# Performance work log

Hardware: AMD Instinct MI355X
Metric: run time of the kernel (lower is better)

Reference implementation:

```python
import jax, jax.numpy as jnp
import numpy as np

N = 50000        # nodes
E = 1_600_000    # edges
IN = 64          # in_feats
H = 128          # h_feats
L = 5            # num_layers
G = 512          # graphs in batch
C = 10           # num_classes


def setup_inputs() -> dict:
    key = jax.random.key(0)
    ks = jax.random.split(key, 12)
    s = 0.05
    x = jax.random.normal(ks[0], (N, IN), jnp.float32)
    edge_index = jax.random.randint(ks[1], (2, E), 0, N, dtype=jnp.int32)
    batch = jnp.sort(jax.random.randint(ks[2], (N,), 0, G, dtype=jnp.int32))
    edge_weight = jax.random.uniform(ks[3], (E,), jnp.float32)
    # GatedGraphConv params: per-layer mixing weight + shared GRUCell
    weight = jax.random.normal(ks[4], (L, H, H), jnp.float32) * s
    w_ih = jax.random.normal(ks[5], (3 * H, H), jnp.float32) * s
    w_hh = jax.random.normal(ks[6], (3 * H, H), jnp.float32) * s
    b_ih = jax.random.normal(ks[7], (3 * H,), jnp.float32) * s
    b_hh = jax.random.normal(ks[8], (3 * H,), jnp.float32) * s
    # MLP head
    dense1_w = jax.random.normal(ks[9], (4 * H, H), jnp.float32) * s
    dense1_b = jnp.zeros((4 * H,), jnp.float32)
    dense2_w = jax.random.normal(ks[10], (C, 4 * H), jnp.float32) * s
    dense2_b = jnp.zeros((C,), jnp.float32)
    return dict(x=x, edge_index=edge_index, batch=batch, edge_weight=edge_weight,
                weight=weight, w_ih=w_ih, w_hh=w_hh, b_ih=b_ih, b_hh=b_hh,
                dense1_w=dense1_w, dense1_b=dense1_b,
                dense2_w=dense2_w, dense2_b=dense2_b)


def _gru_cell(m, h, w_ih, w_hh, b_ih, b_hh):
    # torch.nn.GRUCell(input=m, hidden=h)
    gi = m @ w_ih.T + b_ih
    gh = h @ w_hh.T + b_hh
    i_r, i_z, i_n = jnp.split(gi, 3, axis=-1)
    h_r, h_z, h_n = jnp.split(gh, 3, axis=-1)
    r = jax.nn.sigmoid(i_r + h_r)
    z = jax.nn.sigmoid(i_z + h_z)
    n = jnp.tanh(i_n + r * h_n)
    return (1.0 - z) * n + z * h


def reference(x, edge_index, batch, edge_weight, weight, w_ih, w_hh, b_ih, b_hh,
              dense1_w, dense1_b, dense2_w, dense2_b):
    src, dst = edge_index[0], edge_index[1]
    # pad in_feats -> h_feats (PyG GatedGraphConv)
    h = jnp.pad(x, ((0, 0), (0, H - IN)))
    for l in range(L):
        m = h @ weight[l]                          # [N, H]
        msg = m[src] * edge_weight[:, None]        # gather + edge gating [E, H]
        agg = jax.ops.segment_sum(msg, dst, num_segments=N)  # scatter-add
        h = _gru_cell(agg, h, w_ih, w_hh, b_ih, b_hh)
    pooled = jax.ops.segment_max(h, batch, num_segments=G)   # global max pool [G, H]
    # dropout is identity in eval mode
    hid = jax.nn.relu(pooled @ dense1_w.T + dense1_b)
    out = hid @ dense2_w.T + dense2_b
    return out
```

## Files before the change

### kernel.cpp

```cpp
#include <hip/hip_runtime.h>
#include <hip/hip_bf16.h>

#define NN 50000
#define NE 1600000
#define FIN 64
#define H 128
#define NL 5
#define NG 512
#define NC 10

typedef __attribute__((ext_vector_type(8))) short short8;
typedef __attribute__((ext_vector_type(4))) float f32x4;

#define OFF_H2A   0
#define OFF_H2B   3200000
#define OFF_CUR   6400000
#define OFF_OFF   6450176
#define OFF_CSR   6500352
#define OFF_POOL  8900352
#define OFF_FWF   8965888
#define OFF_FWHH  9088768

__device__ __forceinline__ short rne_bf16(float f){
    unsigned u = __float_as_uint(f);
    unsigned r = (u + 0x7FFFu + ((u >> 16) & 1u)) >> 16;
    return (short)r;
}
__device__ __forceinline__ float bf_lo(unsigned v){ return __uint_as_float(v << 16); }
__device__ __forceinline__ float bf_hi(unsigned v){ return __uint_as_float(v & 0xFFFF0000u); }


__global__ void k_hist(const int* __restrict__ ei, int* __restrict__ cnt){
    int e = blockIdx.x*256 + threadIdx.x;
    if (e < NE) atomicAdd(&cnt[ei[NE + e]], 1);
}

__global__ void k_scan(int* __restrict__ cur, int* __restrict__ off){
    __shared__ int s[1024];
    int t = threadIdx.x;
    const int CH = 49;
    int base = t*CH;
    int m = (NN + 1) - base; if (m > CH) m = CH; if (m < 0) m = 0;
    int sum = 0;
    for (int i = 0; i < m; ++i) sum += (cur[base + i] + 15) & ~15;
    s[t] = sum; __syncthreads();
    for (int o = 1; o < 1024; o <<= 1){
        int v = (t >= o) ? s[t - o] : 0; __syncthreads();
        s[t] += v; __syncthreads();
    }
    int run = s[t] - sum;
    for (int i = 0; i < m; ++i){
        int c = (cur[base + i] + 15) & ~15;
        off[base + i] = run;
        cur[base + i] = run;
        run += c;
    }
}

__global__ void k_fill(const int* __restrict__ ei, const float* __restrict__ ew,
                       int* __restrict__ cur, unsigned* __restrict__ csr){
    int e = blockIdx.x*256 + threadIdx.x;
    if (e >= NE) return;
    int src = ei[e], dst = ei[NE + e];
    int pos = atomicAdd(&cur[dst], 1);
    csr[pos] = (unsigned)src | (((unsigned)(ushort)rne_bf16(ew[e])) << 16);
}


__global__ void k_pad(const float* __restrict__ x, ushort* __restrict__ h2a){
    int idx = blockIdx.x*256 + threadIdx.x;
    int n = idx >> 4, f8 = idx & 15;
    short8 v;
    if (f8 < 8){
        float4 a = *(const float4*)(x + n*FIN + f8*8);
        float4 b = *(const float4*)(x + n*FIN + f8*8 + 4);
        v[0]=rne_bf16(a.x); v[1]=rne_bf16(a.y); v[2]=rne_bf16(a.z); v[3]=rne_bf16(a.w);
        v[4]=rne_bf16(b.x); v[5]=rne_bf16(b.y); v[6]=rne_bf16(b.z); v[7]=rne_bf16(b.w);
    } else {
        v[0]=0; v[1]=0; v[2]=0; v[3]=0; v[4]=0; v[5]=0; v[6]=0; v[7]=0;
    }
    *(short8*)(h2a + idx*8) = v;
}

__global__ void k_fuse(const float* __restrict__ W, const float* __restrict__ wih,
                       short* __restrict__ fwf){
    int idx = blockIdx.x*256 + threadIdx.x;
    int l = idx / 49152;
    int r = idx % 49152;
    int k = r / 384, n = r % 384;
    const float4* wl = (const float4*)(W + l*16384 + k*128);
    const float4* wi = (const float4*)(wih + n*128);
    float acc = 0.f;
    #pragma unroll 8
    for (int c = 0; c < 32; ++c){
        float4 a = wl[c], b = wi[c];
        acc += a.x*b.x + a.y*b.y + a.z*b.z + a.w*b.w;
    }
    int lane = ((k>>3)&3)*16 + (n&15);
    fwf[l*49152 + (((n>>4)*4 + (k>>5))*64 + lane)*8 + (k&7)] = rne_bf16(acc);
}

__global__ void k_cvt_whh(const float* __restrict__ whh, short* __restrict__ fwhh){
    int idx = blockIdx.x*256 + threadIdx.x;
    int k = idx / 384, n = idx % 384;
    float v = whh[n*128 + k];
    int lane = ((k>>3)&3)*16 + (n&15);
    fwhh[(((n>>4)*4 + (k>>5))*64 + lane)*8 + (k&7)] = rne_bf16(v);
}

__global__ void k_init_pool(unsigned* __restrict__ p){
    p[blockIdx.x*256 + threadIdx.x] = 0x007FFFFFu;
}

__global__ __launch_bounds__(512)
void k_layer(const ushort* __restrict__ h2r, ushort* __restrict__ h2w,
             const int* __restrict__ off, const unsigned* __restrict__ csr,
             const short* __restrict__ fwf, const short* __restrict__ fwhh,
             const float* __restrict__ b_ih, const float* __restrict__ b_hh,
             const int* __restrict__ batch, unsigned* __restrict__ pooled,
             int last){
    __shared__ ushort tl[16*136];
    int tid = threadIdx.x;
    int n0 = blockIdx.x * 16;
    int wave = tid >> 6, lane = tid & 63;
    int lane_lo = lane & 15, quad = lane >> 4;
    int grp = lane >> 4, fl = lane & 15;

    for (int sub = 0; sub < 2; ++sub){
        int node = n0 + wave*2 + sub;
        int start = __builtin_amdgcn_readfirstlane(off[node]);
        int end   = __builtin_amdgcn_readfirstlane(off[node + 1]);
        float a0=0.f,a1=0.f,a2=0.f,a3=0.f,a4=0.f,a5=0.f,a6=0.f,a7=0.f;
        const ushort* hb = h2r + fl*8;
        for (int i = start; i < end; i += 16){
            uint4 c = *(const uint4*)(csr + i + grp*4);
            uint4 v0 = *(const uint4*)(hb + (c.x & 0xFFFFu)*H);
            uint4 v1 = *(const uint4*)(hb + (c.y & 0xFFFFu)*H);
            uint4 v2 = *(const uint4*)(hb + (c.z & 0xFFFFu)*H);
            uint4 v3 = *(const uint4*)(hb + (c.w & 0xFFFFu)*H);
            float w0 = bf_hi(c.x), w1 = bf_hi(c.y), w2 = bf_hi(c.z), w3 = bf_hi(c.w);
            a0 += w0*bf_lo(v0.x); a1 += w0*bf_hi(v0.x); a2 += w0*bf_lo(v0.y); a3 += w0*bf_hi(v0.y);
            a4 += w0*bf_lo(v0.z); a5 += w0*bf_hi(v0.z); a6 += w0*bf_lo(v0.w); a7 += w0*bf_hi(v0.w);
            a0 += w1*bf_lo(v1.x); a1 += w1*bf_hi(v1.x); a2 += w1*bf_lo(v1.y); a3 += w1*bf_hi(v1.y);
            a4 += w1*bf_lo(v1.z); a5 += w1*bf_hi(v1.z); a6 += w1*bf_lo(v1.w); a7 += w1*bf_hi(v1.w);
            a0 += w2*bf_lo(v2.x); a1 += w2*bf_hi(v2.x); a2 += w2*bf_lo(v2.y); a3 += w2*bf_hi(v2.y);
            a4 += w2*bf_lo(v2.z); a5 += w2*bf_hi(v2.z); a6 += w2*bf_lo(v2.w); a7 += w2*bf_hi(v2.w);
            a0 += w3*bf_lo(v3.x); a1 += w3*bf_hi(v3.x); a2 += w3*bf_lo(v3.y); a3 += w3*bf_hi(v3.y);
            a4 += w3*bf_lo(v3.z); a5 += w3*bf_hi(v3.z); a6 += w3*bf_lo(v3.w); a7 += w3*bf_hi(v3.w);
        }
        a0 += __shfl_xor(a0,16); a1 += __shfl_xor(a1,16); a2 += __shfl_xor(a2,16); a3 += __shfl_xor(a3,16);
        a4 += __shfl_xor(a4,16); a5 += __shfl_xor(a5,16); a6 += __shfl_xor(a6,16); a7 += __shfl_xor(a7,16);
        a0 += __shfl_xor(a0,32); a1 += __shfl_xor(a1,32); a2 += __shfl_xor(a2,32); a3 += __shfl_xor(a3,32);
        a4 += __shfl_xor(a4,32); a5 += __shfl_xor(a5,32); a6 += __shfl_xor(a6,32); a7 += __shfl_xor(a7,32);
        if (lane < 16){
            short8 hbv;
            hbv[0]=rne_bf16(a0); hbv[1]=rne_bf16(a1); hbv[2]=rne_bf16(a2); hbv[3]=rne_bf16(a3);
            hbv[4]=rne_bf16(a4); hbv[5]=rne_bf16(a5); hbv[6]=rne_bf16(a6); hbv[7]=rne_bf16(a7);
            *(short8*)(tl + (wave*2 + sub)*136 + fl*8) = hbv;
        }
    }
    __syncthreads();

    f32x4 ai[3], ah[3];
    #pragma unroll
    for (int i = 0; i < 3; ++i){ ai[i] = (f32x4){0.f,0.f,0.f,0.f}; ah[i] = (f32x4){0.f,0.f,0.f,0.f}; }

    const ushort* arow_t = tl + lane_lo*136;
    const ushort* arow_h = h2r + (size_t)(n0 + lane_lo)*H;
    #pragma unroll
    for (int kt = 0; kt < 4; ++kt){
        short8 at  = *(const short8*)(arow_t + kt*32 + quad*8);
        short8 ahh = *(const short8*)(arow_h + kt*32 + quad*8);
        #pragma unroll
        for (int s = 0; s < 3; ++s){
            int tile = (s*8 + wave)*4 + kt;
            short8 bi = *(const short8*)(fwf  + tile*512 + lane*8);
            short8 bh = *(const short8*)(fwhh + tile*512 + lane*8);
            ai[s] = __builtin_amdgcn_mfma_f32_16x16x32_bf16(at,  bi, ai[s], 0, 0, 0);
            ah[s] = __builtin_amdgcn_mfma_f32_16x16x32_bf16(ahh, bh, ah[s], 0, 0, 0);
        }
    }

    {
        int j = wave*16 + lane_lo;
        float bir = b_ih[j], biz = b_ih[128 + j], bin_ = b_ih[256 + j];
        float bhr = b_hh[j], bhz = b_hh[128 + j], bhn  = b_hh[256 + j];
        #pragma unroll
        for (int r = 0; r < 4; ++r){
            int row = n0 + quad*4 + r;
            float gir = ai[0][r] + bir, ghr = ah[0][r] + bhr;
            float giz = ai[1][r] + biz, ghz = ah[1][r] + bhz;
            float gin = ai[2][r] + bin_, ghn = ah[2][r] + bhn;
            float rr = 1.f/(1.f + __expf(-(gir + ghr)));
            float zz = 1.f/(1.f + __expf(-(giz + ghz)));
            float nn = tanhf(gin + rr*ghn);
            float ho = __uint_as_float(((unsigned)h2r[(size_t)row*H + j]) << 16);
            float hv = (1.f - zz)*nn + zz*ho;
            if (!last){
                h2w[(size_t)row*H + j] = (ushort)rne_bf16(hv);
            } else {
                int g = batch[row];
                unsigned u = __float_as_uint(hv);
                u = (u & 0x80000000u) ? ~u : (u | 0x80000000u);
                atomicMax(pooled + g*H + j, u);
            }
        }
    }
}


__global__ void k_head(const unsigned* __restrict__ pooled,
                       const float* __restrict__ d1w, const float* __restrict__ d1b,
                       const float* __restrict__ d2w, const float* __restrict__ d2b,
                       float* __restrict__ out){
    __shared__ float sp[128];
    __shared__ float shid[512];
    int g = blockIdx.x, tid = threadIdx.x;
    if (tid < 128){
        unsigned u = pooled[g*H + tid];
        sp[tid] = __uint_as_float((u & 0x80000000u) ? (u ^ 0x80000000u) : ~u);
    }
    __syncthreads();
    for (int o = tid; o < 512; o += 256){
        float acc = d1b[o];
        for (int k = 0; k < H; ++k) acc += sp[k] * d1w[o*H + k];
        shid[o] = fmaxf(acc, 0.f);
    }
    __syncthreads();
    if (tid < NC){
        float acc = d2b[tid];
        for (int o = 0; o < 512; ++o) acc += shid[o] * d2w[tid*512 + o];
        out[g*NC + tid] = acc;
    }
}

extern "C" void kernel_launch(void* const* d_in, const int* in_sizes, int n_in,
                              void* d_out, int out_size, void* d_ws, size_t ws_size,
                              hipStream_t stream){
    const float* x     = (const float*)d_in[0];
    const int*   ei    = (const int*)d_in[1];
    const int*   batch = (const int*)d_in[2];
    const float* ew    = (const float*)d_in[3];
    const float* W     = (const float*)d_in[4];
    const float* wih   = (const float*)d_in[5];
    const float* whh   = (const float*)d_in[6];
    const float* bih   = (const float*)d_in[7];
    const float* bhh   = (const float*)d_in[8];
    const float* d1w   = (const float*)d_in[9];
    const float* d1b   = (const float*)d_in[10];
    const float* d2w   = (const float*)d_in[11];
    const float* d2b   = (const float*)d_in[12];
    float* out = (float*)d_out;

    float*  ws  = (float*)d_ws;
    ushort* h2a = (ushort*)(ws + OFF_H2A);
    ushort* h2b = (ushort*)(ws + OFF_H2B);
    int*    cur = (int*)(ws + OFF_CUR);
    int*    off = (int*)(ws + OFF_OFF);
    unsigned* csr = (unsigned*)(ws + OFF_CSR);
    unsigned* pooled = (unsigned*)(ws + OFF_POOL);
    short*  fwf  = (short*)(ws + OFF_FWF);
    short*  fwhh = (short*)(ws + OFF_FWHH);

    hipMemsetAsync(cur, 0, 50176*sizeof(int), stream);
    hipMemsetAsync(csr, 0, 2400000*sizeof(unsigned), stream);
    k_hist<<<6250, 256, 0, stream>>>(ei, cur);
    k_scan<<<1, 1024, 0, stream>>>(cur, off);
    k_fill<<<6250, 256, 0, stream>>>(ei, ew, cur, csr);

    k_fuse<<<960, 256, 0, stream>>>(W, wih, fwf);
    k_cvt_whh<<<192, 256, 0, stream>>>(whh, fwhh);
    k_pad<<<3125, 256, 0, stream>>>(x, h2a);
    k_init_pool<<<256, 256, 0, stream>>>(pooled);

    for (int l = 0; l < NL; ++l){
        ushort* h2r = (l & 1) ? h2b : h2a;
        ushort* h2w = (l & 1) ? h2a : h2b;
        k_layer<<<3125, 512, 0, stream>>>(h2r, h2w, off, csr,
                                          fwf + (size_t)l*49152, fwhh, bih, bhh,
                                          batch, pooled, (l == NL-1) ? 1 : 0);
    }

    k_head<<<NG, 256, 0, stream>>>(pooled, d1w, d1b, d2w, d2b, out);
}
```

Measured before the change: 864.5 us.

## Process 64 nodes per block to reuse GRU weights and shrink CSR padding

Each block of the fused layer kernel now handles 64 nodes instead of 16, with four 16-row MFMA tiles sharing each loaded weight fragment. The block's own h rows are staged in LDS once for the hidden-side GEMM and the GRU update. CSR segment padding drops from 16 to 4 entries per node, with a bounds guard in the gather loop so fewer padded edges are read. The trade-offs are more accumulator registers and LDS per block, fewer blocks in flight, and tail handling for the last partial block.

```diff
diff --git a/kernel.cpp b/kernel.cpp
--- a/kernel.cpp
+++ b/kernel.cpp
@@ -8,6 +8,8 @@
 #define NL 5
 #define NG 512
 #define NC 10
+#define NPB 64
+#define NBLK 782
 
 typedef __attribute__((ext_vector_type(8))) short short8;
 typedef __attribute__((ext_vector_type(4))) float f32x4;
@@ -29,6 +31,10 @@
 __device__ __forceinline__ float bf_lo(unsigned v){ return __uint_as_float(v << 16); }
 __device__ __forceinline__ float bf_hi(unsigned v){ return __uint_as_float(v & 0xFFFF0000u); }
 
+#define GACC(vv, wt, P) \
+    P##0 += wt*bf_lo(vv.x); P##1 += wt*bf_hi(vv.x); P##2 += wt*bf_lo(vv.y); P##3 += wt*bf_hi(vv.y); \
+    P##4 += wt*bf_lo(vv.z); P##5 += wt*bf_hi(vv.z); P##6 += wt*bf_lo(vv.w); P##7 += wt*bf_hi(vv.w);
+
 
 __global__ void k_hist(const int* __restrict__ ei, int* __restrict__ cnt){
     int e = blockIdx.x*256 + threadIdx.x;
@@ -42,7 +48,7 @@
     int base = t*CH;
     int m = (NN + 1) - base; if (m > CH) m = CH; if (m < 0) m = 0;
     int sum = 0;
-    for (int i = 0; i < m; ++i) sum += (cur[base + i] + 15) & ~15;
+    for (int i = 0; i < m; ++i) sum += (cur[base + i] + 3) & ~3;
     s[t] = sum; __syncthreads();
     for (int o = 1; o < 1024; o <<= 1){
         int v = (t >= o) ? s[t - o] : 0; __syncthreads();
@@ -50,7 +56,7 @@
     }
     int run = s[t] - sum;
     for (int i = 0; i < m; ++i){
-        int c = (cur[base + i] + 15) & ~15;
+        int c = (cur[base + i] + 3) & ~3;
         off[base + i] = run;
         cur[base + i] = run;
         run += c;
@@ -119,65 +125,84 @@
              const float* __restrict__ b_ih, const float* __restrict__ b_hh,
              const int* __restrict__ batch, unsigned* __restrict__ pooled,
              int last){
-    __shared__ ushort tl[16*136];
+    __shared__ ushort tl[64*136];
+    __shared__ ushort th[64*136];
     int tid = threadIdx.x;
-    int n0 = blockIdx.x * 16;
+    int n0 = blockIdx.x * NPB;
     int wave = tid >> 6, lane = tid & 63;
     int lane_lo = lane & 15, quad = lane >> 4;
     int grp = lane >> 4, fl = lane & 15;
 
-    for (int sub = 0; sub < 2; ++sub){
-        int node = n0 + wave*2 + sub;
-        int start = __builtin_amdgcn_readfirstlane(off[node]);
-        int end   = __builtin_amdgcn_readfirstlane(off[node + 1]);
-        float a0=0.f,a1=0.f,a2=0.f,a3=0.f,a4=0.f,a5=0.f,a6=0.f,a7=0.f;
+    {
+        int row = tid >> 3, chunk = tid & 7;
+        int grow = n0 + row;
+        uint4 v0 = {0u,0u,0u,0u}, v1 = {0u,0u,0u,0u};
+        if (grow < NN){
+            v0 = *(const uint4*)(h2r + (size_t)grow*H + chunk*8);
+            v1 = *(const uint4*)(h2r + (size_t)grow*H + (chunk + 8)*8);
+        }
+        *(uint4*)(th + row*136 + chunk*8) = v0;
+        *(uint4*)(th + row*136 + (chunk + 8)*8) = v1;
+    }
+
+    for (int sub = 0; sub < 8; ++sub){
+        int node = n0 + wave*8 + sub;
+        int start = 0, end = 0;
+        if (node < NN){
+            start = __builtin_amdgcn_readfirstlane(off[node]);
+            end   = __builtin_amdgcn_readfirstlane(off[node + 1]);
+        }
+        float A0=0.f,A1=0.f,A2=0.f,A3=0.f,A4=0.f,A5=0.f,A6=0.f,A7=0.f;
         const ushort* hb = h2r + fl*8;
         for (int i = start; i < end; i += 16){
-            uint4 c = *(const uint4*)(csr + i + grp*4);
-            uint4 v0 = *(const uint4*)(hb + (c.x & 0xFFFFu)*H);
-            uint4 v1 = *(const uint4*)(hb + (c.y & 0xFFFFu)*H);
-            uint4 v2 = *(const uint4*)(hb + (c.z & 0xFFFFu)*H);
-            uint4 v3 = *(const uint4*)(hb + (c.w & 0xFFFFu)*H);
-            float w0 = bf_hi(c.x), w1 = bf_hi(c.y), w2 = bf_hi(c.z), w3 = bf_hi(c.w);
-            a0 += w0*bf_lo(v0.x); a1 += w0*bf_hi(v0.x); a2 += w0*bf_lo(v0.y); a3 += w0*bf_hi(v0.y);
-            a4 += w0*bf_lo(v0.z); a5 += w0*bf_hi(v0.z); a6 += w0*bf_lo(v0.w); a7 += w0*bf_hi(v0.w);
-            a0 += w1*bf_lo(v1.x); a1 += w1*bf_hi(v1.x); a2 += w1*bf_lo(v1.y); a3 += w1*bf_hi(v1.y);
-            a4 += w1*bf_lo(v1.z); a5 += w1*bf_hi(v1.z); a6 += w1*bf_lo(v1.w); a7 += w1*bf_hi(v1.w);
-            a0 += w2*bf_lo(v2.x); a1 += w2*bf_hi(v2.x); a2 += w2*bf_lo(v2.y); a3 += w2*bf_hi(v2.y);
-            a4 += w2*bf_lo(v2.z); a5 += w2*bf_hi(v2.z); a6 += w2*bf_lo(v2.w); a7 += w2*bf_hi(v2.w);
-            a0 += w3*bf_lo(v3.x); a1 += w3*bf_hi(v3.x); a2 += w3*bf_lo(v3.y); a3 += w3*bf_hi(v3.y);
-            a4 += w3*bf_lo(v3.z); a5 += w3*bf_hi(v3.z); a6 += w3*bf_lo(v3.w); a7 += w3*bf_hi(v3.w);
-        }
-        a0 += __shfl_xor(a0,16); a1 += __shfl_xor(a1,16); a2 += __shfl_xor(a2,16); a3 += __shfl_xor(a3,16);
-        a4 += __shfl_xor(a4,16); a5 += __shfl_xor(a5,16); a6 += __shfl_xor(a6,16); a7 += __shfl_xor(a7,16);
-        a0 += __shfl_xor(a0,32); a1 += __shfl_xor(a1,32); a2 += __shfl_xor(a2,32); a3 += __shfl_xor(a3,32);
-        a4 += __shfl_xor(a4,32); a5 += __shfl_xor(a5,32); a6 += __shfl_xor(a6,32); a7 += __shfl_xor(a7,32);
+            int ii = i + grp*4;
+            if (ii < end){
+                uint4 c = *(const uint4*)(csr + ii);
+                uint4 v0 = *(const uint4*)(hb + (c.x & 0xFFFFu)*H);
+                uint4 v1 = *(const uint4*)(hb + (c.y & 0xFFFFu)*H);
+                uint4 v2 = *(const uint4*)(hb + (c.z & 0xFFFFu)*H);
+                uint4 v3 = *(const uint4*)(hb + (c.w & 0xFFFFu)*H);
+                float w0 = bf_hi(c.x), w1 = bf_hi(c.y), w2 = bf_hi(c.z), w3 = bf_hi(c.w);
+                GACC(v0, w0, A) GACC(v1, w1, A) GACC(v2, w2, A) GACC(v3, w3, A)
+            }
+        }
+        A0 += __shfl_xor(A0,16); A1 += __shfl_xor(A1,16); A2 += __shfl_xor(A2,16); A3 += __shfl_xor(A3,16);
+        A4 += __shfl_xor(A4,16); A5 += __shfl_xor(A5,16); A6 += __shfl_xor(A6,16); A7 += __shfl_xor(A7,16);
+        A0 += __shfl_xor(A0,32); A1 += __shfl_xor(A1,32); A2 += __shfl_xor(A2,32); A3 += __shfl_xor(A3,32);
+        A4 += __shfl_xor(A4,32); A5 += __shfl_xor(A5,32); A6 += __shfl_xor(A6,32); A7 += __shfl_xor(A7,32);
         if (lane < 16){
-            short8 hbv;
-            hbv[0]=rne_bf16(a0); hbv[1]=rne_bf16(a1); hbv[2]=rne_bf16(a2); hbv[3]=rne_bf16(a3);
-            hbv[4]=rne_bf16(a4); hbv[5]=rne_bf16(a5); hbv[6]=rne_bf16(a6); hbv[7]=rne_bf16(a7);
-            *(short8*)(tl + (wave*2 + sub)*136 + fl*8) = hbv;
+            short8 hv;
+            hv[0]=rne_bf16(A0); hv[1]=rne_bf16(A1); hv[2]=rne_bf16(A2); hv[3]=rne_bf16(A3);
+            hv[4]=rne_bf16(A4); hv[5]=rne_bf16(A5); hv[6]=rne_bf16(A6); hv[7]=rne_bf16(A7);
+            *(short8*)(tl + (wave*8 + sub)*136 + fl*8) = hv;
         }
     }
     __syncthreads();
 
-    f32x4 ai[3], ah[3];
+    f32x4 ai[4][3], ah[4][3];
     #pragma unroll
-    for (int i = 0; i < 3; ++i){ ai[i] = (f32x4){0.f,0.f,0.f,0.f}; ah[i] = (f32x4){0.f,0.f,0.f,0.f}; }
-
-    const ushort* arow_t = tl + lane_lo*136;
-    const ushort* arow_h = h2r + (size_t)(n0 + lane_lo)*H;
+    for (int rt = 0; rt < 4; ++rt)
+        #pragma unroll
+        for (int s = 0; s < 3; ++s){ ai[rt][s] = (f32x4){0.f,0.f,0.f,0.f}; ah[rt][s] = (f32x4){0.f,0.f,0.f,0.f}; }
+
     #pragma unroll
     for (int kt = 0; kt < 4; ++kt){
-        short8 at  = *(const short8*)(arow_t + kt*32 + quad*8);
-        short8 ahh = *(const short8*)(arow_h + kt*32 + quad*8);
+        short8 at[4], ahh[4];
+        #pragma unroll
+        for (int rt = 0; rt < 4; ++rt){
+            at[rt]  = *(const short8*)(tl + (rt*16 + lane_lo)*136 + kt*32 + quad*8);
+            ahh[rt] = *(const short8*)(th + (rt*16 + lane_lo)*136 + kt*32 + quad*8);
+        }
         #pragma unroll
         for (int s = 0; s < 3; ++s){
             int tile = (s*8 + wave)*4 + kt;
             short8 bi = *(const short8*)(fwf  + tile*512 + lane*8);
             short8 bh = *(const short8*)(fwhh + tile*512 + lane*8);
-            ai[s] = __builtin_amdgcn_mfma_f32_16x16x32_bf16(at,  bi, ai[s], 0, 0, 0);
-            ah[s] = __builtin_amdgcn_mfma_f32_16x16x32_bf16(ahh, bh, ah[s], 0, 0, 0);
+            #pragma unroll
+            for (int rt = 0; rt < 4; ++rt){
+                ai[rt][s] = __builtin_amdgcn_mfma_f32_16x16x32_bf16(at[rt],  bi, ai[rt][s], 0, 0, 0);
+                ah[rt][s] = __builtin_amdgcn_mfma_f32_16x16x32_bf16(ahh[rt], bh, ah[rt][s], 0, 0, 0);
+            }
         }
     }
 
@@ -186,23 +211,29 @@
         float bir = b_ih[j], biz = b_ih[128 + j], bin_ = b_ih[256 + j];
         float bhr = b_hh[j], bhz = b_hh[128 + j], bhn  = b_hh[256 + j];
         #pragma unroll
-        for (int r = 0; r < 4; ++r){
-            int row = n0 + quad*4 + r;
-            float gir = ai[0][r] + bir, ghr = ah[0][r] + bhr;
-            float giz = ai[1][r] + biz, ghz = ah[1][r] + bhz;
-            float gin = ai[2][r] + bin_, ghn = ah[2][r] + bhn;
-            float rr = 1.f/(1.f + __expf(-(gir + ghr)));
-            float zz = 1.f/(1.f + __expf(-(giz + ghz)));
-            float nn = tanhf(gin + rr*ghn);
-            float ho = __uint_as_float(((unsigned)h2r[(size_t)row*H + j]) << 16);
-            float hv = (1.f - zz)*nn + zz*ho;
-            if (!last){
-                h2w[(size_t)row*H + j] = (ushort)rne_bf16(hv);
-            } else {
-                int g = batch[row];
-                unsigned u = __float_as_uint(hv);
-                u = (u & 0x80000000u) ? ~u : (u | 0x80000000u);
-                atomicMax(pooled + g*H + j, u);
+        for (int rt = 0; rt < 4; ++rt){
+            #pragma unroll
+            for (int r = 0; r < 4; ++r){
+                int lrow = rt*16 + quad*4 + r;
+                int row = n0 + lrow;
+                float gir = ai[rt][0][r] + bir, ghr = ah[rt][0][r] + bhr;
+                float giz = ai[rt][1][r] + biz, ghz = ah[rt][1][r] + bhz;
+                float gin = ai[rt][2][r] + bin_, ghn = ah[rt][2][r] + bhn;
+                float rr = 1.f/(1.f + __expf(-(gir + ghr)));
+                float zz = 1.f/(1.f + __expf(-(giz + ghz)));
+                float nn = tanhf(gin + rr*ghn);
+                float ho = __uint_as_float(((unsigned)th[lrow*136 + j]) << 16);
+                float hv = (1.f - zz)*nn + zz*ho;
+                if (row < NN){
+                    if (!last){
+                        h2w[(size_t)row*H + j] = (ushort)rne_bf16(hv);
+                    } else {
+                        int g = batch[row];
+                        unsigned u = __float_as_uint(hv);
+                        u = (u & 0x80000000u) ? ~u : (u | 0x80000000u);
+                        atomicMax(pooled + g*H + j, u);
+                    }
+                }
             }
         }
     }
@@ -276,7 +307,7 @@
     for (int l = 0; l < NL; ++l){
         ushort* h2r = (l & 1) ? h2b : h2a;
         ushort* h2w = (l & 1) ? h2a : h2b;
-        k_layer<<<3125, 512, 0, stream>>>(h2r, h2w, off, csr,
+        k_layer<<<NBLK, 512, 0, stream>>>(h2r, h2w, off, csr,
                                           fwf + (size_t)l*49152, fwhh, bih, bhh,
                                           batch, pooled, (l == NL-1) ? 1 : 0);
     }
```

New measurement: 1.114 ms. +28.9%, slower.
